# Kernel optimization log

Hardware: AMD Instinct MI355X
Metric: run time of the kernel (lower is better)

## Reference

```python
import jax, jax.numpy as jnp
import numpy as np

B, T, H = 32, 2048, 1024


def setup_inputs() -> dict:
    key = jax.random.key(0)
    ks = jax.random.split(key, 5)
    s = 1.0 / np.sqrt(H)
    return {
        "x": jax.random.normal(ks[0], (B, H), dtype=jnp.float32),
        "context": jax.random.normal(ks[1], (B, T, H), dtype=jnp.float32),
        "mask": jnp.ones((B, T), dtype=bool),
        "Wq": jax.random.normal(ks[2], (H, H), dtype=jnp.float32) * s,
        "bq": jnp.zeros((H,), dtype=jnp.float32),
        "Wm": jax.random.normal(ks[3], (H, H), dtype=jnp.float32) * s,
        "bm": jnp.zeros((H,), dtype=jnp.float32),
        "v": jax.random.normal(ks[4], (H,), dtype=jnp.float32) * s,
    }


def reference(x, context, mask, Wq, bq, Wm, bm, v):
    # h_x: [B,1,H]; h_c: [B,T,H]  (mask is unused, matching the original module)
    h_x = (x @ Wq.T + bq)[:, None, :]
    h_c = jnp.einsum('bth,oh->bto', context, Wm) + bm
    # score: [B,T] = tanh(h_x + h_c) . v, then softmax over T
    score = jax.nn.softmax(jnp.einsum('bth,h->bt', jnp.tanh(h_x + h_c), v), axis=-1)
    # context-weighted sum over T -> [B,H]
    c = jnp.einsum('bth,bt->bh', context, score)
    return (c, score)
```

## Files before the change

### kernel.cpp

```cpp
#include <hip/hip_runtime.h>
#include <math.h>

#define B_ 32
#define T_ 2048
#define H_ 1024

typedef __bf16 bf16x8 __attribute__((ext_vector_type(8)));
typedef float f32x4 __attribute__((ext_vector_type(4)));

__device__ __forceinline__ unsigned short f2bf(float f) {
  unsigned int u = __float_as_uint(f);
  u += 0x7fffu + ((u >> 16) & 1u);
  return (unsigned short)(u >> 16);
}

__device__ __forceinline__ float bf2f(unsigned short s) {
  return __uint_as_float(((unsigned int)s) << 16);
}

__device__ __forceinline__ float fast_tanh(float x) {
  float e = __expf(2.0f * x);
  return 1.0f - __fdividef(2.0f, e + 1.0f);
}

__global__ void prep_kernel(const float* __restrict__ x, const float* __restrict__ Wq,
                            const float* __restrict__ bq, const float* __restrict__ bm,
                            const float* __restrict__ Wm, const float* __restrict__ ctx,
                            float* __restrict__ hxb, unsigned short* __restrict__ wmb,
                            unsigned short* __restrict__ ctxb,
                            float* __restrict__ logits, float* __restrict__ outc) {
  int blk = blockIdx.x, tid = threadIdx.x;
  if (blk < 128) {
    int idx = (blk << 8) + tid;
    int b = idx >> 10, o = idx & (H_ - 1);
    const float4* xr = (const float4*)(x + b * H_);
    const float4* wr = (const float4*)(Wq + o * H_);
    float s = 0.f;
#pragma unroll 8
    for (int h = 0; h < H_ / 4; ++h) {
      float4 xv = xr[h], wv = wr[h];
      s += xv.x * wv.x + xv.y * wv.y + xv.z * wv.z + xv.w * wv.w;
    }
    hxb[idx] = s + bq[o] + bm[o];
  } else if (blk < 1152) {
    int i = ((blk - 128) << 10) + (tid << 2);
    float4 wv = *(const float4*)(Wm + i);
    *(ushort4*)(wmb + i) = make_ushort4(f2bf(wv.x), f2bf(wv.y), f2bf(wv.z), f2bf(wv.w));
  } else if (blk < 1248) {
    int zblk = blk - 1152;
    if (zblk < 64) {
      *(float4*)(logits + (zblk << 10) + (tid << 2)) = (float4){0.f, 0.f, 0.f, 0.f};
    } else {
      *(float4*)(outc + ((zblk - 64) << 10) + (tid << 2)) = (float4){0.f, 0.f, 0.f, 0.f};
    }
  } else {
    size_t i = ((size_t)(blk - 1248) << 11) + ((size_t)tid << 3);
    float4 a = *(const float4*)(ctx + i);
    float4 c = *(const float4*)(ctx + i + 4);
    *(ushort4*)(ctxb + i) = make_ushort4(f2bf(a.x), f2bf(a.y), f2bf(a.z), f2bf(a.w));
    *(ushort4*)(ctxb + i + 4) = make_ushort4(f2bf(c.x), f2bf(c.y), f2bf(c.z), f2bf(c.w));
  }
}

template <bool PRECONV>
__global__ __launch_bounds__(256) void score_kernel(
    const float* __restrict__ ctxf, const unsigned short* __restrict__ ctxb,
    const unsigned short* __restrict__ wmb,
    const float* __restrict__ hxb, const float* __restrict__ v,
    float* logits) {
  __shared__ __align__(16) unsigned short As[128][72];
  __shared__ float part[128];

  int tid = threadIdx.x;
  int xx = blockIdx.x;
  int ot = xx >> 9;
  int bt = xx & 511;
  int b = bt >> 4;
  int t0 = (bt & 15) << 7;
  int o0 = ot << 7;
  if (tid < 128) part[tid] = 0.f;

  int lane = tid & 63;
  int wave = tid >> 6;
  int wm = (wave >> 1) << 6;
  int wn = (wave & 1) << 6;
  int q = lane >> 4;
  int m = lane & 15;
  const unsigned short* cb = PRECONV ? (ctxb + ((size_t)b * T_ + t0) * H_) : nullptr;
  const float* cf = PRECONV ? nullptr : (ctxf + ((size_t)b * T_ + t0) * H_);

  int ar = tid >> 3;
  int ac = (tid & 7) << 3;

  f32x4 acc[4][4];
#pragma unroll
  for (int i = 0; i < 4; ++i)
#pragma unroll
    for (int j = 0; j < 4; ++j) acc[i][j] = (f32x4){0.f, 0.f, 0.f, 0.f};

  for (int k0 = 0; k0 < H_; k0 += 64) {
    __syncthreads();
#pragma unroll
    for (int rep = 0; rep < 4; ++rep) {
      int row = ar + (rep << 5);
      if (PRECONV) {
        *(uint4*)(&As[row][ac]) = *(const uint4*)(cb + (size_t)row * H_ + k0 + ac);
      } else {
        const float* src = cf + (size_t)row * H_ + k0 + ac;
        float4 f0 = *(const float4*)(src);
        float4 f1 = *(const float4*)(src + 4);
        *(ushort4*)(&As[row][ac]) =
            make_ushort4(f2bf(f0.x), f2bf(f0.y), f2bf(f0.z), f2bf(f0.w));
        *(ushort4*)(&As[row][ac + 4]) =
            make_ushort4(f2bf(f1.x), f2bf(f1.y), f2bf(f1.z), f2bf(f1.w));
      }
    }
    __syncthreads();
#pragma unroll
    for (int kk = 0; kk < 2; ++kk) {
      bf16x8 af[4], bfr[4];
      const unsigned short* wp =
          wmb + (size_t)(o0 + wn + m) * H_ + k0 + (kk << 5) + (q << 3);
#pragma unroll
      for (int j = 0; j < 4; ++j)
        bfr[j] = *(const bf16x8*)(wp + ((size_t)(j << 4) * H_));
#pragma unroll
      for (int i = 0; i < 4; ++i)
        af[i] = *(const bf16x8*)(&As[wm + (i << 4) + m][(kk << 5) + (q << 3)]);
#pragma unroll
      for (int i = 0; i < 4; ++i)
#pragma unroll
        for (int j = 0; j < 4; ++j)
          acc[i][j] = __builtin_amdgcn_mfma_f32_16x16x32_bf16(af[i], bfr[j], acc[i][j], 0, 0, 0);
    }
  }

  float hb[4], vv[4];
#pragma unroll
  for (int j = 0; j < 4; ++j) {
    int o = o0 + wn + (j << 4) + m;
    hb[j] = hxb[(b << 10) + o];
    vv[j] = v[o];
  }
#pragma unroll
  for (int i = 0; i < 4; ++i) {
#pragma unroll
    for (int r = 0; r < 4; ++r) {
      float s = 0.f;
#pragma unroll
      for (int j = 0; j < 4; ++j) s += fast_tanh(acc[i][j][r] + hb[j]) * vv[j];
      s += __shfl_xor(s, 1);
      s += __shfl_xor(s, 2);
      s += __shfl_xor(s, 4);
      s += __shfl_xor(s, 8);
      if (m == 0) atomicAdd(&part[wm + (i << 4) + (q << 2) + r], s);
    }
  }
  __syncthreads();
  if (tid < 128) atomicAdd(&logits[b * T_ + t0 + tid], part[tid]);
}

template <bool PRECONV>
__global__ void wsum_kernel(const float* __restrict__ ctxf, const unsigned short* __restrict__ ctxb,
                            const float* __restrict__ logits,
                            float* __restrict__ score, float* __restrict__ outc) {
  int tid = threadIdx.x;
  int b = blockIdx.z;
  int tch = blockIdx.y << 8;
  __shared__ float wred[4];
  __shared__ float sc[256];

  const float* lb = logits + b * T_;
  float l[8];
  float mx = -3.4e38f;
#pragma unroll
  for (int i = 0; i < 8; ++i) { l[i] = lb[tid + (i << 8)]; mx = fmaxf(mx, l[i]); }
#pragma unroll
  for (int d = 1; d < 64; d <<= 1) mx = fmaxf(mx, __shfl_xor(mx, d));
  if ((tid & 63) == 0) wred[tid >> 6] = mx;
  __syncthreads();
  mx = fmaxf(fmaxf(wred[0], wred[1]), fmaxf(wred[2], wred[3]));
  __syncthreads();
  float e[8];
  float se = 0.f;
#pragma unroll
  for (int i = 0; i < 8; ++i) { e[i] = __expf(l[i] - mx); se += e[i]; }
#pragma unroll
  for (int d = 1; d < 64; d <<= 1) se += __shfl_xor(se, d);
  if ((tid & 63) == 0) wred[tid >> 6] = se;
  __syncthreads();
  se = wred[0] + wred[1] + wred[2] + wred[3];
  float inv = 1.0f / se;
  sc[tid] = e[blockIdx.y] * inv;
  if (blockIdx.x == 0 && blockIdx.y == 0) {
#pragma unroll
    for (int i = 0; i < 8; ++i) score[b * T_ + tid + (i << 8)] = e[i] * inv;
  }
  __syncthreads();

  int h = (blockIdx.x << 9) + (tid << 1);
  float s0 = 0.f, s1 = 0.f;
  if (PRECONV) {
    const unsigned short* cp = ctxb + ((size_t)b * T_ + tch) * H_ + h;
#pragma unroll 4
    for (int t = 0; t < 256; ++t) {
      unsigned int u = *(const unsigned int*)(cp + (size_t)t * H_);
      s0 += bf2f((unsigned short)(u & 0xffffu)) * sc[t];
      s1 += bf2f((unsigned short)(u >> 16)) * sc[t];
    }
  } else {
    const float* cp = ctxf + ((size_t)b * T_ + tch) * H_ + h;
#pragma unroll 4
    for (int t = 0; t < 256; ++t) {
      float2 f = *(const float2*)(cp + (size_t)t * H_);
      s0 += f.x * sc[t];
      s1 += f.y * sc[t];
    }
  }
  atomicAdd(&outc[(b << 10) + h], s0);
  atomicAdd(&outc[(b << 10) + h + 1], s1);
}

extern "C" void kernel_launch(void* const* d_in, const int* in_sizes, int n_in,
                              void* d_out, int out_size, void* d_ws, size_t ws_size,
                              hipStream_t stream) {
  const float* x   = (const float*)d_in[0];
  const float* ctx = (const float*)d_in[1];
  const float* Wq  = (const float*)d_in[3];
  const float* bq  = (const float*)d_in[4];
  const float* Wm  = (const float*)d_in[5];
  const float* bm  = (const float*)d_in[6];
  const float* v   = (const float*)d_in[7];

  float* out_c = (float*)d_out;
  float* out_s = out_c + B_ * H_;

  char* ws = (char*)d_ws;
  float* hxb = (float*)ws;
  unsigned short* wmb = (unsigned short*)(ws + 131072);
  float* logits = (float*)(ws + 131072 + 2097152);
  size_t off_ctxb = 131072 + 2097152 + 262144;
  unsigned short* ctxb = (unsigned short*)(ws + off_ctxb);
  size_t need = off_ctxb + (size_t)B_ * T_ * H_ * 2;
  bool preconv = (ws_size >= need);

  int prep_blocks = preconv ? (1248 + 32768) : 1248;
  prep_kernel<<<dim3(prep_blocks), 256, 0, stream>>>(x, Wq, bq, bm, Wm, ctx, hxb, wmb,
                                                     preconv ? ctxb : nullptr, logits, out_c);
  if (preconv) {
    score_kernel<true><<<dim3(4096), 256, 0, stream>>>(ctx, ctxb, wmb, hxb, v, logits);
    wsum_kernel<true><<<dim3(H_ / 512, T_ / 256, B_), 256, 0, stream>>>(ctx, ctxb, logits, out_s, out_c);
  } else {
    score_kernel<false><<<dim3(4096), 256, 0, stream>>>(ctx, ctxb, wmb, hxb, v, logits);
    wsum_kernel<false><<<dim3(H_ / 512, T_ / 256, B_), 256, 0, stream>>>(ctx, ctxb, logits, out_s, out_c);
  }
}
```

Measured before the change: 767.0 us.

## Stage Wm tiles in LDS via async global-to-LDS loads with XOR swizzle, re-split prep and wsum

The score GEMM now loads both the context tile and the Wm tile into swizzled shared memory using global_load_lds async 16-byte copies. Previously the Wm fragments were read directly from global memory by each wave. The XOR swizzle replaces padding to avoid LDS bank conflicts. The hx projection in prep now uses one wave per output with a shuffle reduction, which adds parallelism, and wsum is regridded to cover the full H per block with wider vector loads. These changes add complexity and depend on the alignment and ordering semantics of the LDS-direct load intrinsic.

```diff
diff --git a/kernel.cpp b/kernel.cpp
--- a/kernel.cpp
+++ b/kernel.cpp
@@ -21,6 +21,14 @@
 __device__ __forceinline__ float fast_tanh(float x) {
   float e = __expf(2.0f * x);
   return 1.0f - __fdividef(2.0f, e + 1.0f);
+}
+
+__device__ __forceinline__ void async16(const void* g, void* l) {
+  typedef const __attribute__((address_space(1))) void* gvp;
+  typedef __attribute__((address_space(3))) void* lvp;
+  __builtin_amdgcn_global_load_lds((gvp)(unsigned long long)g,
+                                   (lvp)(unsigned int)(unsigned long long)l,
+                                   16, 0, 0);
 }
 
 __global__ void prep_kernel(const float* __restrict__ x, const float* __restrict__ Wq,
@@ -30,31 +38,35 @@
                             unsigned short* __restrict__ ctxb,
                             float* __restrict__ logits, float* __restrict__ outc) {
   int blk = blockIdx.x, tid = threadIdx.x;
-  if (blk < 128) {
-    int idx = (blk << 8) + tid;
-    int b = idx >> 10, o = idx & (H_ - 1);
-    const float4* xr = (const float4*)(x + b * H_);
-    const float4* wr = (const float4*)(Wq + o * H_);
+  if (blk < 8192) {
+    int wave = tid >> 6, lane = tid & 63;
+    int pair = (blk << 2) + wave;
+    int b = pair >> 10, o = pair & (H_ - 1);
+    const float4* wr = (const float4*)(Wq + (size_t)o * H_);
+    const float4* xr = (const float4*)(x + (size_t)b * H_);
     float s = 0.f;
-#pragma unroll 8
-    for (int h = 0; h < H_ / 4; ++h) {
-      float4 xv = xr[h], wv = wr[h];
-      s += xv.x * wv.x + xv.y * wv.y + xv.z * wv.z + xv.w * wv.w;
-    }
-    hxb[idx] = s + bq[o] + bm[o];
-  } else if (blk < 1152) {
-    int i = ((blk - 128) << 10) + (tid << 2);
+#pragma unroll
+    for (int s4 = 0; s4 < 4; ++s4) {
+      float4 wv = wr[(s4 << 6) + lane];
+      float4 xv = xr[(s4 << 6) + lane];
+      s += wv.x * xv.x + wv.y * xv.y + wv.z * xv.z + wv.w * xv.w;
+    }
+#pragma unroll
+    for (int d = 1; d < 64; d <<= 1) s += __shfl_xor(s, d);
+    if (lane == 0) hxb[(b << 10) + o] = s + bq[o] + bm[o];
+  } else if (blk < 9216) {
+    int i = ((blk - 8192) << 10) + (tid << 2);
     float4 wv = *(const float4*)(Wm + i);
     *(ushort4*)(wmb + i) = make_ushort4(f2bf(wv.x), f2bf(wv.y), f2bf(wv.z), f2bf(wv.w));
-  } else if (blk < 1248) {
-    int zblk = blk - 1152;
+  } else if (blk < 9312) {
+    int zblk = blk - 9216;
     if (zblk < 64) {
       *(float4*)(logits + (zblk << 10) + (tid << 2)) = (float4){0.f, 0.f, 0.f, 0.f};
     } else {
       *(float4*)(outc + ((zblk - 64) << 10) + (tid << 2)) = (float4){0.f, 0.f, 0.f, 0.f};
     }
   } else {
-    size_t i = ((size_t)(blk - 1248) << 11) + ((size_t)tid << 3);
+    size_t i = ((size_t)(blk - 9312) << 11) + ((size_t)tid << 3);
     float4 a = *(const float4*)(ctx + i);
     float4 c = *(const float4*)(ctx + i + 4);
     *(ushort4*)(ctxb + i) = make_ushort4(f2bf(a.x), f2bf(a.y), f2bf(a.z), f2bf(a.w));
@@ -68,7 +80,8 @@
     const unsigned short* __restrict__ wmb,
     const float* __restrict__ hxb, const float* __restrict__ v,
     float* logits) {
-  __shared__ __align__(16) unsigned short As[128][72];
+  __shared__ __align__(16) unsigned short As[128 * 64];
+  __shared__ __align__(16) unsigned short Bs[128 * 64];
   __shared__ float part[128];
 
   int tid = threadIdx.x;
@@ -86,11 +99,10 @@
   int wn = (wave & 1) << 6;
   int q = lane >> 4;
   int m = lane & 15;
+
   const unsigned short* cb = PRECONV ? (ctxb + ((size_t)b * T_ + t0) * H_) : nullptr;
   const float* cf = PRECONV ? nullptr : (ctxf + ((size_t)b * T_ + t0) * H_);
-
-  int ar = tid >> 3;
-  int ac = (tid & 7) << 3;
+  const unsigned short* wb = wmb + (size_t)o0 * H_;
 
   f32x4 acc[4][4];
 #pragma unroll
@@ -101,32 +113,43 @@
   for (int k0 = 0; k0 < H_; k0 += 64) {
     __syncthreads();
 #pragma unroll
-    for (int rep = 0; rep < 4; ++rep) {
-      int row = ar + (rep << 5);
+    for (int i = 0; i < 4; ++i) {
+      int ig = (wave << 2) + i;
+      int p = (ig << 6) + lane;
+      int row = p >> 3;
+      int gl = (p & 7) ^ (row & 7);
+      size_t goff = (size_t)row * H_ + k0 + (gl << 3);
       if (PRECONV) {
-        *(uint4*)(&As[row][ac]) = *(const uint4*)(cb + (size_t)row * H_ + k0 + ac);
+        async16(cb + goff, (char*)As + ((size_t)ig << 10));
       } else {
-        const float* src = cf + (size_t)row * H_ + k0 + ac;
+        int arow = (tid >> 3) + (i << 5);
+        int agl = tid & 7;
+        int agp = agl ^ (arow & 7);
+        const float* src = cf + (size_t)arow * H_ + k0 + (agl << 3);
         float4 f0 = *(const float4*)(src);
         float4 f1 = *(const float4*)(src + 4);
-        *(ushort4*)(&As[row][ac]) =
-            make_ushort4(f2bf(f0.x), f2bf(f0.y), f2bf(f0.z), f2bf(f0.w));
-        *(ushort4*)(&As[row][ac + 4]) =
-            make_ushort4(f2bf(f1.x), f2bf(f1.y), f2bf(f1.z), f2bf(f1.w));
+        unsigned short* dst = As + (arow << 6) + (agp << 3);
+        *(ushort4*)(dst) = make_ushort4(f2bf(f0.x), f2bf(f0.y), f2bf(f0.z), f2bf(f0.w));
+        *(ushort4*)(dst + 4) = make_ushort4(f2bf(f1.x), f2bf(f1.y), f2bf(f1.z), f2bf(f1.w));
       }
+      async16(wb + goff, (char*)Bs + ((size_t)ig << 10));
     }
     __syncthreads();
 #pragma unroll
     for (int kk = 0; kk < 2; ++kk) {
       bf16x8 af[4], bfr[4];
-      const unsigned short* wp =
-          wmb + (size_t)(o0 + wn + m) * H_ + k0 + (kk << 5) + (q << 3);
-#pragma unroll
-      for (int j = 0; j < 4; ++j)
-        bfr[j] = *(const bf16x8*)(wp + ((size_t)(j << 4) * H_));
-#pragma unroll
-      for (int i = 0; i < 4; ++i)
-        af[i] = *(const bf16x8*)(&As[wm + (i << 4) + m][(kk << 5) + (q << 3)]);
+#pragma unroll
+      for (int i = 0; i < 4; ++i) {
+        int row = wm + (i << 4) + m;
+        int gp = ((kk << 2) + q) ^ (row & 7);
+        af[i] = *(const bf16x8*)(As + (row << 6) + (gp << 3));
+      }
+#pragma unroll
+      for (int j = 0; j < 4; ++j) {
+        int row = wn + (j << 4) + m;
+        int gp = ((kk << 2) + q) ^ (row & 7);
+        bfr[j] = *(const bf16x8*)(Bs + (row << 6) + (gp << 3));
+      }
 #pragma unroll
       for (int i = 0; i < 4; ++i)
 #pragma unroll
@@ -165,10 +188,10 @@
                             const float* __restrict__ logits,
                             float* __restrict__ score, float* __restrict__ outc) {
   int tid = threadIdx.x;
-  int b = blockIdx.z;
-  int tch = blockIdx.y << 8;
+  int b = blockIdx.y;
+  int tc = blockIdx.x << 7;
   __shared__ float wred[4];
-  __shared__ float sc[256];
+  __shared__ float sc[128];
 
   const float* lb = logits + b * T_;
   float l[8];
@@ -191,34 +214,44 @@
   __syncthreads();
   se = wred[0] + wred[1] + wred[2] + wred[3];
   float inv = 1.0f / se;
-  sc[tid] = e[blockIdx.y] * inv;
-  if (blockIdx.x == 0 && blockIdx.y == 0) {
+#pragma unroll
+  for (int i = 0; i < 8; ++i) {
+    int tg = tid + (i << 8);
+    if ((tg >> 7) == (int)blockIdx.x) sc[tg & 127] = e[i] * inv;
+  }
+  if (blockIdx.x == 0) {
 #pragma unroll
     for (int i = 0; i < 8; ++i) score[b * T_ + tid + (i << 8)] = e[i] * inv;
   }
   __syncthreads();
 
-  int h = (blockIdx.x << 9) + (tid << 1);
-  float s0 = 0.f, s1 = 0.f;
+  int h = tid << 2;
+  float s0 = 0.f, s1 = 0.f, s2 = 0.f, s3 = 0.f;
   if (PRECONV) {
-    const unsigned short* cp = ctxb + ((size_t)b * T_ + tch) * H_ + h;
+    const unsigned short* cp = ctxb + ((size_t)b * T_ + tc) * H_ + h;
 #pragma unroll 4
-    for (int t = 0; t < 256; ++t) {
-      unsigned int u = *(const unsigned int*)(cp + (size_t)t * H_);
-      s0 += bf2f((unsigned short)(u & 0xffffu)) * sc[t];
-      s1 += bf2f((unsigned short)(u >> 16)) * sc[t];
+    for (int t = 0; t < 128; ++t) {
+      uint2 u = *(const uint2*)(cp + (size_t)t * H_);
+      float w = sc[t];
+      s0 += bf2f((unsigned short)(u.x & 0xffffu)) * w;
+      s1 += bf2f((unsigned short)(u.x >> 16)) * w;
+      s2 += bf2f((unsigned short)(u.y & 0xffffu)) * w;
+      s3 += bf2f((unsigned short)(u.y >> 16)) * w;
     }
   } else {
-    const float* cp = ctxf + ((size_t)b * T_ + tch) * H_ + h;
+    const float* cp = ctxf + ((size_t)b * T_ + tc) * H_ + h;
 #pragma unroll 4
-    for (int t = 0; t < 256; ++t) {
-      float2 f = *(const float2*)(cp + (size_t)t * H_);
-      s0 += f.x * sc[t];
-      s1 += f.y * sc[t];
-    }
-  }
-  atomicAdd(&outc[(b << 10) + h], s0);
-  atomicAdd(&outc[(b << 10) + h + 1], s1);
+    for (int t = 0; t < 128; ++t) {
+      float4 f = *(const float4*)(cp + (size_t)t * H_);
+      float w = sc[t];
+      s0 += f.x * w; s1 += f.y * w; s2 += f.z * w; s3 += f.w * w;
+    }
+  }
+  float* op = outc + (b << 10) + h;
+  atomicAdd(op + 0, s0);
+  atomicAdd(op + 1, s1);
+  atomicAdd(op + 2, s2);
+  atomicAdd(op + 3, s3);
 }
 
 extern "C" void kernel_launch(void* const* d_in, const int* in_sizes, int n_in,
@@ -244,14 +277,14 @@
   size_t need = off_ctxb + (size_t)B_ * T_ * H_ * 2;
   bool preconv = (ws_size >= need);
 
-  int prep_blocks = preconv ? (1248 + 32768) : 1248;
+  int prep_blocks = preconv ? (9312 + 32768) : 9312;
   prep_kernel<<<dim3(prep_blocks), 256, 0, stream>>>(x, Wq, bq, bm, Wm, ctx, hxb, wmb,
                                                      preconv ? ctxb : nullptr, logits, out_c);
   if (preconv) {
     score_kernel<true><<<dim3(4096), 256, 0, stream>>>(ctx, ctxb, wmb, hxb, v, logits);
-    wsum_kernel<true><<<dim3(H_ / 512, T_ / 256, B_), 256, 0, stream>>>(ctx, ctxb, logits, out_s, out_c);
+    wsum_kernel<true><<<dim3(T_ / 128, B_), 256, 0, stream>>>(ctx, ctxb, logits, out_s, out_c);
   } else {
     score_kernel<false><<<dim3(4096), 256, 0, stream>>>(ctx, ctxb, wmb, hxb, v, logits);
-    wsum_kernel<false><<<dim3(H_ / 512, T_ / 256, B_), 256, 0, stream>>>(ctx, ctxb, logits, out_s, out_c);
-  }
-}
+    wsum_kernel<false><<<dim3(T_ / 128, B_), 256, 0, stream>>>(ctx, ctxb, logits, out_s, out_c);
+  }
+}
```

Result: faster. 651.9 us (-15.0%).
